# Optimization experiments

Hardware: AMD Instinct MI355X
Metric: run time of the kernel (lower is better)

The kernel has to match this reference:

```python
import jax, jax.numpy as jnp
import numpy as np

N_HEADS = 16
K_CH = 1024 // N_HEADS  # 64
SCALE = 1.0 / np.sqrt(K_CH)


def setup_inputs() -> dict:
    key = jax.random.key(0)
    ks = jax.random.split(key, 10)
    B, C, T = 4, 1024, 2048
    Cout = 1024
    xavier = lambda k, o, i: jax.random.uniform(k, (o, i), jnp.float32, -1.0, 1.0) * np.sqrt(6.0 / (o + i))
    return {
        "x": jax.random.normal(ks[0], (B, C, T), jnp.float32),
        "c": jax.random.normal(ks[1], (B, C, T), jnp.float32),
        "Wq": xavier(ks[2], C, C), "bq": jnp.zeros((C,), jnp.float32),
        "Wk": xavier(ks[3], C, C), "bk": jnp.zeros((C,), jnp.float32),
        "Wv": xavier(ks[4], C, C), "bv": jnp.zeros((C,), jnp.float32),
        "Wo": xavier(ks[5], Cout, C), "bo": jnp.zeros((Cout,), jnp.float32),
    }


def reference(x, c, Wq, bq, Wk, bk, Wv, bv, Wo, bo):
    B, C, T = x.shape
    H, K = N_HEADS, K_CH
    # 1x1 Conv1d == per-timestep linear: [O,C] @ [B,C,T] -> [B,O,T]
    q = jnp.einsum('oc,bct->bot', Wq, x) + bq[None, :, None]
    k = jnp.einsum('oc,bct->bot', Wk, c) + bk[None, :, None]
    v = jnp.einsum('oc,bct->bot', Wv, c) + bv[None, :, None]
    # split heads: b (h k) t -> b h k t
    q = q.reshape(B, H, K, T)
    k = k.reshape(B, H, K, -1)
    v = v.reshape(B, H, K, -1)
    scores = jnp.einsum('bhkt,bhks->bhts', q, k) * SCALE  # [B,H,Tt,Ts]
    p = jax.nn.softmax(scores, axis=-1)
    out = jnp.einsum('bhts,bhks->bhkt', p, v)  # b h k t
    out = out.reshape(B, H * K, T)
    return jnp.einsum('oc,bct->bot', Wo, out) + bo[None, :, None]
```

## Files before the change

### kernel.cpp

```cpp
#include <hip/hip_runtime.h>
#include <stdint.h>

typedef __bf16 bf16x8 __attribute__((ext_vector_type(8)));
typedef float f32x4 __attribute__((ext_vector_type(4)));
typedef float f32x16 __attribute__((ext_vector_type(16)));
typedef unsigned u32x2 __attribute__((ext_vector_type(2)));
typedef unsigned u32x4 __attribute__((ext_vector_type(4)));

#define LOG2E 1.44269504088896340736f
#define ATT_SCALE 0.125f
#define CL (ATT_SCALE * LOG2E)
#define SWZ(row, colb) ((colb) ^ (((row) & 7) << 4))

#define GLOAD_LDS16(gp, lp)                                                  \
  __builtin_amdgcn_global_load_lds(                                          \
      (const __attribute__((address_space(1))) void*)(gp),                   \
      (__attribute__((address_space(3))) void*)(lp), 16, 0, 0)

__device__ __forceinline__ unsigned short f2bf(float f) {
  unsigned int x = __float_as_uint(f);
  x += 0x7fffu + ((x >> 16) & 1u);
  return (unsigned short)(x >> 16);
}

__device__ __forceinline__ float fexp2(float x) {
#if __has_builtin(__builtin_amdgcn_exp2f)
  return __builtin_amdgcn_exp2f(x);
#else
  return exp2f(x);
#endif
}

__device__ __forceinline__ unsigned cvtpk(float lo, float hi) {
  unsigned r;
  asm("v_cvt_pk_bf16_f32 %0, %1, %2" : "=v"(r) : "v"(lo), "v"(hi));
  return r;
}

__device__ __forceinline__ u32x2 plswap(unsigned a, unsigned b) {
  asm("v_permlane32_swap_b32 %0, %1" : "+v"(a), "+v"(b));
  u32x2 r;
  r[0] = a;
  r[1] = b;
  return r;
}

__global__ __launch_bounds__(256) void prep_inputs(
    const float* __restrict__ x, const float* __restrict__ c,
    const float* __restrict__ Wq, const float* __restrict__ Wk,
    const float* __restrict__ Wv, const float* __restrict__ Wo,
    unsigned short* __restrict__ xT, unsigned short* __restrict__ cT,
    unsigned short* __restrict__ wqb, unsigned short* __restrict__ wkb,
    unsigned short* __restrict__ wvb, unsigned short* __restrict__ wob) {
  const int C = 1024, T = 2048;
  int z = blockIdx.z;
  if (z >= 8) {
    int sel = z - 8;
    int bi = blockIdx.y * 64 + blockIdx.x;
    if (bi >= 512) return;
    const float* in = sel == 0 ? Wq : sel == 1 ? Wk : sel == 2 ? Wv : Wo;
    unsigned short* out = sel == 0 ? wqb : sel == 1 ? wkb : sel == 2 ? wvb : wob;
    float scale = sel == 0 ? CL : 1.0f;
    int off = (bi * 256 + threadIdx.x) * 8;
    #pragma unroll
    for (int p = 0; p < 2; ++p) {
      float4 v = *(const float4*)(in + off + p * 4);
      ushort4 o;
      o.x = f2bf(v.x * scale); o.y = f2bf(v.y * scale);
      o.z = f2bf(v.z * scale); o.w = f2bf(v.w * scale);
      *(ushort4*)(out + off + p * 4) = o;
    }
    return;
  }
  __shared__ unsigned short tile[32][33];
  const float* in = (z < 4) ? x : c;
  unsigned short* out = (z < 4) ? xT : cT;
  int b = z & 3;
  int t0 = blockIdx.x * 32, c0 = blockIdx.y * 32;
  int tx = threadIdx.x & 31, ty = threadIdx.x >> 5;
  const float* src = in + ((size_t)b * C + c0) * T + t0;
  #pragma unroll
  for (int i = 0; i < 4; ++i) {
    int cc = ty + i * 8;
    tile[cc][tx] = f2bf(src[(size_t)cc * T + tx]);
  }
  __syncthreads();
  unsigned short* dst = out + ((size_t)b * T + t0) * C + c0;
  #pragma unroll
  for (int i = 0; i < 4; ++i) {
    int tt = ty + i * 8;
    dst[(size_t)tt * C + tx] = tile[tx][tt];
  }
}

template <int NT, int OUT_F32>
__device__ __forceinline__ void gemm_core128(
    const unsigned short* __restrict__ A, const unsigned short* __restrict__ B,
    void* __restrict__ Cv, const float* __restrict__ bias, int bias_is_m,
    float bs, int m0, int n0, int ldC) {
  __shared__ __align__(16) char lds[3 * 16384];
  const int tid = threadIdx.x;
  const int l = tid & 63, w = tid >> 6;
  const int g = l >> 4, j = l & 15;
  const int wr = w >> 1, wc = w & 1;

  const int r0 = tid >> 3;
  const int slotp = (tid & 7) ^ (r0 & 7);
  const int mloc = r0 * 2 + (slotp >> 2);
  const int kg = slotp & 3;
  const unsigned short* ga0 = A + (size_t)(m0 + mloc) * 1024 + kg * 8;
  const unsigned short* ga1 = A + (size_t)(m0 + 64 + mloc) * 1024 + kg * 8;
  const unsigned short* gb0 = B + (size_t)(n0 + mloc) * 1024 + kg * 8;
  const unsigned short* gb1 = B + (size_t)(n0 + 64 + mloc) * 1024 + kg * 8;

  auto stage = [&](char* buf) {
    GLOAD_LDS16(ga0, buf + tid * 16);
    GLOAD_LDS16(ga1, buf + 4096 + tid * 16);
    GLOAD_LDS16(gb0, buf + 8192 + tid * 16);
    GLOAD_LDS16(gb1, buf + 12288 + tid * 16);
    ga0 += 32; ga1 += 32; gb0 += 32; gb1 += 32;
  };

  f32x4 acc[4][4] = {};

  stage(lds);
  stage(lds + 16384);

  char* bufc = lds;
  char* bufs = lds + 2 * 16384;

  for (int t = 0; t < NT; ++t) {
    if (t == NT - 1) asm volatile("s_waitcnt vmcnt(0)" ::: "memory");
    else             asm volatile("s_waitcnt vmcnt(4)" ::: "memory");
    __builtin_amdgcn_s_barrier();
    asm volatile("" ::: "memory");
    if (t < NT - 2) stage(bufs);

    bf16x8 af[4], bfr[4];
    #pragma unroll
    for (int mf = 0; mf < 4; ++mf) {
      int m = wr * 64 + mf * 16 + j;
      int rp = m >> 1;
      int cb = ((m & 1) * 64 + g * 16) ^ ((rp & 7) << 4);
      af[mf] = *(const bf16x8*)(bufc + rp * 128 + cb);
    }
    #pragma unroll
    for (int nf = 0; nf < 4; ++nf) {
      int n = wc * 64 + nf * 16 + j;
      int rp = n >> 1;
      int cb = ((n & 1) * 64 + g * 16) ^ ((rp & 7) << 4);
      bfr[nf] = *(const bf16x8*)(bufc + 8192 + rp * 128 + cb);
    }
    #pragma unroll
    for (int mf = 0; mf < 4; ++mf)
      #pragma unroll
      for (int nf = 0; nf < 4; ++nf)
        acc[mf][nf] = __builtin_amdgcn_mfma_f32_16x16x32_bf16(af[mf], bfr[nf], acc[mf][nf], 0, 0, 0);

    bufc += 16384; if (bufc == lds + 49152) bufc = lds;
    bufs += 16384; if (bufs == lds + 49152) bufs = lds;
  }

  #pragma unroll
  for (int mf = 0; mf < 4; ++mf) {
    #pragma unroll
    for (int rr = 0; rr < 4; ++rr) {
      int m = m0 + wr * 64 + mf * 16 + g * 4 + rr;
      float bm = bias_is_m ? bias[m] * bs : 0.f;
      #pragma unroll
      for (int nf = 0; nf < 4; ++nf) {
        int n = n0 + wc * 64 + nf * 16 + j;
        float val = acc[mf][nf][rr] + bm + (bias_is_m ? 0.f : bias[n] * bs);
        if (OUT_F32) ((float*)Cv)[(size_t)m * ldC + n] = val;
        else ((unsigned short*)Cv)[(size_t)m * ldC + n] = f2bf(val);
      }
    }
  }
}

__global__ __launch_bounds__(256, 3) void qkv_gemm3(
    const unsigned short* __restrict__ xT, const unsigned short* __restrict__ cT,
    const unsigned short* __restrict__ wq, const unsigned short* __restrict__ wk,
    const unsigned short* __restrict__ wv,
    const float* __restrict__ bq, const float* __restrict__ bk,
    const float* __restrict__ bv,
    unsigned short* __restrict__ QT, unsigned short* __restrict__ KT,
    unsigned short* __restrict__ Vb) {
  const size_t sBT = (size_t)2048 * 1024;
  const int id = (blockIdx.x & 7) * 192 + (blockIdx.x >> 3);
  const int op = id >> 9;
  const int r = id & 511;
  const int z = r >> 7;
  const unsigned short *A, *B;
  unsigned short* Cp;
  const float* bias;
  int m0, n0, ldC, bias_is_m;
  float bs;
  if (op == 2) {
    n0 = (r & 15) * 128; m0 = ((r >> 4) & 7) * 128;
    A = wv; B = cT + z * sBT; Cp = Vb + z * (size_t)1024 * 2048;
    bias = bv; ldC = 2048; bias_is_m = 1; bs = 1.0f;
  } else {
    n0 = (r & 7) * 128; m0 = ((r >> 3) & 15) * 128;
    A = (op == 0 ? xT : cT) + z * sBT;
    B = (op == 0 ? wq : wk);
    Cp = (op == 0 ? QT : KT) + z * sBT;
    bias = (op == 0 ? bq : bk); ldC = 1024; bias_is_m = 0;
    bs = (op == 0) ? CL : 1.0f;
  }
  gemm_core128<32, 0>(A, B, Cp, bias, bias_is_m, bs, m0, n0, ldC);
}

__global__ __launch_bounds__(256, 3) void gemm_out3(
    const unsigned short* __restrict__ Wo, const unsigned short* __restrict__ OT,
    float* __restrict__ Out, const float* __restrict__ bias) {
  const size_t sBT = (size_t)2048 * 1024;
  const int id = (blockIdx.x & 7) * 64 + (blockIdx.x >> 3);
  const int z = id >> 7;
  const int m0 = ((id >> 4) & 7) * 128, n0 = (id & 15) * 128;
  gemm_core128<32, 1>(Wo, OT + z * sBT, Out + z * (size_t)1024 * 2048,
                      bias, 1, 1.0f, m0, n0, 2048);
}

__global__ __launch_bounds__(256, 3) void attn_kernel6(const unsigned short* __restrict__ QT,
                                                       const unsigned short* __restrict__ KT,
                                                       const unsigned short* __restrict__ V,
                                                       unsigned short* __restrict__ OT) {
  __shared__ __align__(16) char kv[3][16384];

  const int fid = blockIdx.x;
  const int xcd = fid & 7, idx = fid >> 3;
  const int bh = ((idx & 7) << 3) | xcd;
  const int tblk = idx >> 3;
  const int b = bh >> 4, h = bh & 15;

  const int tid = threadIdx.x;
  const int w = tid >> 6, l = tid & 63, lo5 = l & 31, hi = l >> 5;
  const int tq0 = tblk * 128 + w * 32;

  bf16x8 q[4];
  {
    const unsigned short* Qb = QT + ((size_t)(b * 2048 + tq0 + lo5)) * 1024 + h * 64 + hi * 8;
    #pragma unroll
    for (int kb = 0; kb < 4; ++kb) q[kb] = *(const bf16x8*)(Qb + kb * 16);
  }

  f32x16 o[2] = {};
  f32x16 ol = {};

  const unsigned one2 = 0x3F803F80u;
  const bf16x8 ones = __builtin_bit_cast(bf16x8, (u32x4){one2, one2, one2, one2});

  const int srow0 = tid >> 3, sslot = tid & 7;
  const int ch0 = sslot ^ (srow0 & 7);
  const int ch1 = sslot ^ ((32 + srow0) & 7);
  const unsigned short* kp0 = KT + ((size_t)(b * 2048 + srow0)) * 1024 + h * 64 + ch0 * 8;
  const unsigned short* kp1 = KT + ((size_t)(b * 2048 + 32 + srow0)) * 1024 + h * 64 + ch1 * 8;
  const unsigned short* vp0 = V + ((size_t)(b * 1024 + h * 64 + srow0)) * 2048 + ch0 * 8;
  const unsigned short* vp1 = V + ((size_t)(b * 1024 + h * 64 + 32 + srow0)) * 2048 + ch1 * 8;

  auto stage = [&](char* buf) {
    GLOAD_LDS16(kp0, buf + tid * 16);
    GLOAD_LDS16(kp1, buf + 4096 + tid * 16);
    GLOAD_LDS16(vp0, buf + 8192 + tid * 16);
    GLOAD_LDS16(vp1, buf + 12288 + tid * 16);
    kp0 += 64 * 1024; kp1 += 64 * 1024;
    vp0 += 64; vp1 += 64;
  };

  stage(kv[0]);
  stage(kv[1]);

  char* bufc = kv[0];
  char* bufs = kv[2];

  for (int t = 0; t < 32; ++t) {
    if (t == 31) asm volatile("s_waitcnt vmcnt(0)" ::: "memory");
    else         asm volatile("s_waitcnt vmcnt(4)" ::: "memory");
    __builtin_amdgcn_s_barrier();
    asm volatile("" ::: "memory");
    if (t < 30) stage(bufs);

    const char* Ks = bufc;
    const char* Vs = bufc + 8192;

    f32x16 p0 = {}, p1 = {};
    #pragma unroll
    for (int kb = 0; kb < 4; ++kb) {
      int r0 = lo5, r1 = 32 + lo5;
      bf16x8 ka0 = *(const bf16x8*)(Ks + r0 * 128 + SWZ(r0, kb * 32 + hi * 16));
      bf16x8 ka1 = *(const bf16x8*)(Ks + r1 * 128 + SWZ(r1, kb * 32 + hi * 16));
      p0 = __builtin_amdgcn_mfma_f32_32x32x16_bf16(ka0, q[kb], p0, 0, 0, 0);
      p1 = __builtin_amdgcn_mfma_f32_32x32x16_bf16(ka1, q[kb], p1, 0, 0, 0);
    }

    #pragma unroll
    for (int r = 0; r < 16; ++r) p0[r] = fexp2(p0[r]);
    #pragma unroll
    for (int r = 0; r < 16; ++r) p1[r] = fexp2(p1[r]);

    u32x4 pa[4];
    {
      u32x2 ra = plswap(cvtpk(p0[0], p0[1]), cvtpk(p0[4], p0[5]));
      u32x2 rb = plswap(cvtpk(p0[2], p0[3]), cvtpk(p0[6], p0[7]));
      pa[0] = (u32x4){ra[0], rb[0], ra[1], rb[1]};
      u32x2 rc = plswap(cvtpk(p0[8], p0[9]), cvtpk(p0[12], p0[13]));
      u32x2 rd = plswap(cvtpk(p0[10], p0[11]), cvtpk(p0[14], p0[15]));
      pa[1] = (u32x4){rc[0], rd[0], rc[1], rd[1]};
      u32x2 re = plswap(cvtpk(p1[0], p1[1]), cvtpk(p1[4], p1[5]));
      u32x2 rf = plswap(cvtpk(p1[2], p1[3]), cvtpk(p1[6], p1[7]));
      pa[2] = (u32x4){re[0], rf[0], re[1], rf[1]};
      u32x2 rg = plswap(cvtpk(p1[8], p1[9]), cvtpk(p1[12], p1[13]));
      u32x2 rh = plswap(cvtpk(p1[10], p1[11]), cvtpk(p1[14], p1[15]));
      pa[3] = (u32x4){rg[0], rh[0], rg[1], rh[1]};
    }

    #pragma unroll
    for (int sb = 0; sb < 4; ++sb) {
      bf16x8 pab = __builtin_bit_cast(bf16x8, pa[sb]);
      #pragma unroll
      for (int kb2 = 0; kb2 < 2; ++kb2) {
        int row = kb2 * 32 + lo5;
        bf16x8 vb = *(const bf16x8*)(Vs + row * 128 + SWZ(row, sb * 32 + hi * 16));
        o[kb2] = __builtin_amdgcn_mfma_f32_32x32x16_bf16(pab, vb, o[kb2], 0, 0, 0);
      }
      ol = __builtin_amdgcn_mfma_f32_32x32x16_bf16(pab, ones, ol, 0, 0, 0);
    }

    bufc += 16384; if (bufc == kv[0] + 49152) bufc = kv[0];
    bufs += 16384; if (bufs == kv[0] + 49152) bufs = kv[0];
  }

  unsigned short* Ob = OT + ((size_t)(b * 2048 + tq0)) * 1024 + h * 64 + lo5;
  #pragma unroll
  for (int r = 0; r < 16; ++r) {
    int srow = (r & 3) + 8 * (r >> 2) + 4 * hi;
    float inv = 1.0f / ol[r];
    Ob[(size_t)srow * 1024 + 0]  = f2bf(o[0][r] * inv);
    Ob[(size_t)srow * 1024 + 32] = f2bf(o[1][r] * inv);
  }
}

extern "C" void kernel_launch(void* const* d_in, const int* in_sizes, int n_in,
                              void* d_out, int out_size, void* d_ws, size_t ws_size,
                              hipStream_t stream) {
  const float* x  = (const float*)d_in[0];
  const float* c  = (const float*)d_in[1];
  const float* Wq = (const float*)d_in[2];
  const float* bq = (const float*)d_in[3];
  const float* Wk = (const float*)d_in[4];
  const float* bk = (const float*)d_in[5];
  const float* Wv = (const float*)d_in[6];
  const float* bv = (const float*)d_in[7];
  const float* Wo = (const float*)d_in[8];
  const float* bo = (const float*)d_in[9];

  const size_t MB = 1024 * 1024;
  char* ws = (char*)d_ws;
  unsigned short* wqb = (unsigned short*)(ws + 0 * MB);
  unsigned short* wkb = (unsigned short*)(ws + 2 * MB);
  unsigned short* wvb = (unsigned short*)(ws + 4 * MB);
  unsigned short* wob = (unsigned short*)(ws + 6 * MB);
  unsigned short* xT  = (unsigned short*)(ws + 8 * MB);
  unsigned short* cT  = (unsigned short*)(ws + 24 * MB);
  unsigned short* QT  = (unsigned short*)(ws + 40 * MB);
  unsigned short* KT  = (unsigned short*)(ws + 56 * MB);
  unsigned short* Vb  = (unsigned short*)(ws + 72 * MB);
  unsigned short* OT  = xT;

  prep_inputs<<<dim3(64, 32, 12), 256, 0, stream>>>(x, c, Wq, Wk, Wv, Wo,
                                                    xT, cT, wqb, wkb, wvb, wob);

  qkv_gemm3<<<dim3(1536), 256, 0, stream>>>(xT, cT, wqb, wkb, wvb, bq, bk, bv, QT, KT, Vb);

  attn_kernel6<<<dim3(1024), 256, 0, stream>>>(QT, KT, Vb, OT);

  gemm_out3<<<dim3(512), 256, 0, stream>>>(wob, OT, (float*)d_out, bo);
}
```

Measured before the change: 189.8 us.

## Process two query tiles per wave in attention and compute row sums on VALU

Each attention wave now handles 64 query rows instead of 32. K fragments are loaded from LDS once per step and reused for both query tiles, and the grid is halved to 512 blocks with launch bounds lowered to 2 blocks per CU. The softmax denominator is now accumulated with scalar adds over the exponentials and combined across lane halves through a small shared buffer, replacing the extra MFMA against a ones vector. This cuts LDS reads and MFMA work per output, at the cost of more registers, lower occupancy and fewer blocks to spread across CUs.

After: 181.7 us, median of 2. -4.3%, faster.

```diff
diff --git a/kernel.cpp b/kernel.cpp
--- a/kernel.cpp
+++ b/kernel.cpp
@@ -222,11 +222,12 @@
                       bias, 1, 1.0f, m0, n0, 2048);
 }
 
-__global__ __launch_bounds__(256, 3) void attn_kernel6(const unsigned short* __restrict__ QT,
+__global__ __launch_bounds__(256, 2) void attn_kernel8(const unsigned short* __restrict__ QT,
                                                        const unsigned short* __restrict__ KT,
                                                        const unsigned short* __restrict__ V,
                                                        unsigned short* __restrict__ OT) {
   __shared__ __align__(16) char kv[3][16384];
+  __shared__ float lbuf[4][32];
 
   const int fid = blockIdx.x;
   const int xcd = fid & 7, idx = fid >> 3;
@@ -236,20 +237,20 @@
 
   const int tid = threadIdx.x;
   const int w = tid >> 6, l = tid & 63, lo5 = l & 31, hi = l >> 5;
-  const int tq0 = tblk * 128 + w * 32;
-
-  bf16x8 q[4];
+  const int tq0 = tblk * 256 + w * 64;
+
+  bf16x8 q[2][4];
   {
     const unsigned short* Qb = QT + ((size_t)(b * 2048 + tq0 + lo5)) * 1024 + h * 64 + hi * 8;
     #pragma unroll
-    for (int kb = 0; kb < 4; ++kb) q[kb] = *(const bf16x8*)(Qb + kb * 16);
-  }
-
-  f32x16 o[2] = {};
-  f32x16 ol = {};
-
-  const unsigned one2 = 0x3F803F80u;
-  const bf16x8 ones = __builtin_bit_cast(bf16x8, (u32x4){one2, one2, one2, one2});
+    for (int tb = 0; tb < 2; ++tb)
+      #pragma unroll
+      for (int kb = 0; kb < 4; ++kb)
+        q[tb][kb] = *(const bf16x8*)(Qb + (size_t)tb * 32 * 1024 + kb * 16);
+  }
+
+  f32x16 o[2][2] = {};
+  float lr[2] = {0.f, 0.f};
 
   const int srow0 = tid >> 3, sslot = tid & 7;
   const int ch0 = sslot ^ (srow0 & 7);
@@ -284,60 +285,82 @@
     const char* Ks = bufc;
     const char* Vs = bufc + 8192;
 
-    f32x16 p0 = {}, p1 = {};
-    #pragma unroll
-    for (int kb = 0; kb < 4; ++kb) {
-      int r0 = lo5, r1 = 32 + lo5;
-      bf16x8 ka0 = *(const bf16x8*)(Ks + r0 * 128 + SWZ(r0, kb * 32 + hi * 16));
-      bf16x8 ka1 = *(const bf16x8*)(Ks + r1 * 128 + SWZ(r1, kb * 32 + hi * 16));
-      p0 = __builtin_amdgcn_mfma_f32_32x32x16_bf16(ka0, q[kb], p0, 0, 0, 0);
-      p1 = __builtin_amdgcn_mfma_f32_32x32x16_bf16(ka1, q[kb], p1, 0, 0, 0);
-    }
-
-    #pragma unroll
-    for (int r = 0; r < 16; ++r) p0[r] = fexp2(p0[r]);
-    #pragma unroll
-    for (int r = 0; r < 16; ++r) p1[r] = fexp2(p1[r]);
-
-    u32x4 pa[4];
-    {
+    bf16x8 ka[2][4];
+    #pragma unroll
+    for (int sblk = 0; sblk < 2; ++sblk)
+      #pragma unroll
+      for (int kb = 0; kb < 4; ++kb) {
+        int row = sblk * 32 + lo5;
+        ka[sblk][kb] = *(const bf16x8*)(Ks + row * 128 + SWZ(row, kb * 32 + hi * 16));
+      }
+
+    u32x4 pa[2][4];
+    #pragma unroll
+    for (int tb = 0; tb < 2; ++tb) {
+      f32x16 p0 = {}, p1 = {};
+      #pragma unroll
+      for (int kb = 0; kb < 4; ++kb) {
+        p0 = __builtin_amdgcn_mfma_f32_32x32x16_bf16(ka[0][kb], q[tb][kb], p0, 0, 0, 0);
+        p1 = __builtin_amdgcn_mfma_f32_32x32x16_bf16(ka[1][kb], q[tb][kb], p1, 0, 0, 0);
+      }
+
+      float ls0 = 0.f, ls1 = 0.f, ls2 = 0.f, ls3 = 0.f;
+      #pragma unroll
+      for (int r = 0; r < 16; r += 4) {
+        float e0 = fexp2(p0[r]), e1 = fexp2(p0[r + 1]), e2 = fexp2(p0[r + 2]), e3 = fexp2(p0[r + 3]);
+        p0[r] = e0; p0[r + 1] = e1; p0[r + 2] = e2; p0[r + 3] = e3;
+        ls0 += e0; ls1 += e1; ls2 += e2; ls3 += e3;
+      }
+      #pragma unroll
+      for (int r = 0; r < 16; r += 4) {
+        float e0 = fexp2(p1[r]), e1 = fexp2(p1[r + 1]), e2 = fexp2(p1[r + 2]), e3 = fexp2(p1[r + 3]);
+        p1[r] = e0; p1[r + 1] = e1; p1[r + 2] = e2; p1[r + 3] = e3;
+        ls0 += e0; ls1 += e1; ls2 += e2; ls3 += e3;
+      }
+      lr[tb] += (ls0 + ls1) + (ls2 + ls3);
+
       u32x2 ra = plswap(cvtpk(p0[0], p0[1]), cvtpk(p0[4], p0[5]));
       u32x2 rb = plswap(cvtpk(p0[2], p0[3]), cvtpk(p0[6], p0[7]));
-      pa[0] = (u32x4){ra[0], rb[0], ra[1], rb[1]};
+      pa[tb][0] = (u32x4){ra[0], rb[0], ra[1], rb[1]};
       u32x2 rc = plswap(cvtpk(p0[8], p0[9]), cvtpk(p0[12], p0[13]));
       u32x2 rd = plswap(cvtpk(p0[10], p0[11]), cvtpk(p0[14], p0[15]));
-      pa[1] = (u32x4){rc[0], rd[0], rc[1], rd[1]};
+      pa[tb][1] = (u32x4){rc[0], rd[0], rc[1], rd[1]};
       u32x2 re = plswap(cvtpk(p1[0], p1[1]), cvtpk(p1[4], p1[5]));
       u32x2 rf = plswap(cvtpk(p1[2], p1[3]), cvtpk(p1[6], p1[7]));
-      pa[2] = (u32x4){re[0], rf[0], re[1], rf[1]};
+      pa[tb][2] = (u32x4){re[0], rf[0], re[1], rf[1]};
       u32x2 rg = plswap(cvtpk(p1[8], p1[9]), cvtpk(p1[12], p1[13]));
       u32x2 rh = plswap(cvtpk(p1[10], p1[11]), cvtpk(p1[14], p1[15]));
-      pa[3] = (u32x4){rg[0], rh[0], rg[1], rh[1]};
-    }
-
-    #pragma unroll
-    for (int sb = 0; sb < 4; ++sb) {
-      bf16x8 pab = __builtin_bit_cast(bf16x8, pa[sb]);
+      pa[tb][3] = (u32x4){rg[0], rh[0], rg[1], rh[1]};
+    }
+
+    #pragma unroll
+    for (int sb = 0; sb < 4; ++sb)
       #pragma unroll
       for (int kb2 = 0; kb2 < 2; ++kb2) {
         int row = kb2 * 32 + lo5;
         bf16x8 vb = *(const bf16x8*)(Vs + row * 128 + SWZ(row, sb * 32 + hi * 16));
-        o[kb2] = __builtin_amdgcn_mfma_f32_32x32x16_bf16(pab, vb, o[kb2], 0, 0, 0);
-      }
-      ol = __builtin_amdgcn_mfma_f32_32x32x16_bf16(pab, ones, ol, 0, 0, 0);
-    }
+        o[0][kb2] = __builtin_amdgcn_mfma_f32_32x32x16_bf16(
+            __builtin_bit_cast(bf16x8, pa[0][sb]), vb, o[0][kb2], 0, 0, 0);
+        o[1][kb2] = __builtin_amdgcn_mfma_f32_32x32x16_bf16(
+            __builtin_bit_cast(bf16x8, pa[1][sb]), vb, o[1][kb2], 0, 0, 0);
+      }
 
     bufc += 16384; if (bufc == kv[0] + 49152) bufc = kv[0];
     bufs += 16384; if (bufs == kv[0] + 49152) bufs = kv[0];
   }
 
-  unsigned short* Ob = OT + ((size_t)(b * 2048 + tq0)) * 1024 + h * 64 + lo5;
   #pragma unroll
-  for (int r = 0; r < 16; ++r) {
-    int srow = (r & 3) + 8 * (r >> 2) + 4 * hi;
-    float inv = 1.0f / ol[r];
-    Ob[(size_t)srow * 1024 + 0]  = f2bf(o[0][r] * inv);
-    Ob[(size_t)srow * 1024 + 32] = f2bf(o[1][r] * inv);
+  for (int tb = 0; tb < 2; ++tb) {
+    float lt = lr[tb] + __shfl_xor(lr[tb], 32);
+    if (hi == 0) lbuf[w][lo5] = 1.0f / lt;
+    unsigned short* Ob = OT + ((size_t)(b * 2048 + tq0 + tb * 32)) * 1024 + h * 64 + lo5;
+    #pragma unroll
+    for (int r = 0; r < 16; ++r) {
+      int srow = (r & 3) + 8 * (r >> 2) + 4 * hi;
+      float inv = lbuf[w][srow];
+      Ob[(size_t)srow * 1024 + 0]  = f2bf(o[tb][0][r] * inv);
+      Ob[(size_t)srow * 1024 + 32] = f2bf(o[tb][1][r] * inv);
+    }
   }
 }
 
@@ -373,7 +396,7 @@
 
   qkv_gemm3<<<dim3(1536), 256, 0, stream>>>(xT, cT, wqb, wkb, wvb, bq, bk, bv, QT, KT, Vb);
 
-  attn_kernel6<<<dim3(1024), 256, 0, stream>>>(QT, KT, Vb, OT);
+  attn_kernel8<<<dim3(512), 256, 0, stream>>>(QT, KT, Vb, OT);
 
   gemm_out3<<<dim3(512), 256, 0, stream>>>(wob, OT, (float*)d_out, bo);
 }
```
